# Optimization experiments

Hardware: AMD Instinct MI355X
Metric: run time of the kernel (lower is better)

## Reference

```python
import jax, jax.numpy as jnp
import numpy as np

B, N, M, CIN, COUT = 16, 512, 1024, 7, 64
C = CIN + 1  # density channel prepended
INIT_LS = 0.1


def setup_inputs() -> dict:
    key = jax.random.key(0)
    k1, k2, k3, k4 = jax.random.split(key, 4)
    context_in = jax.random.uniform(k1, (B, N, 1), dtype=jnp.float32)
    context_out = jax.random.normal(k2, (B, N, CIN), dtype=jnp.float32)
    target_in = jax.random.uniform(k3, (B, M, 1), dtype=jnp.float32)
    # learned params: sigma = log(init_length_scale) * ones(C); xavier-normal Linear
    sigma = jnp.full((C,), np.log(INIT_LS), dtype=jnp.float32)
    xavier_std = float(np.sqrt(2.0 / (C + COUT)))
    W = jax.random.normal(k4, (COUT, C), dtype=jnp.float32) * xavier_std
    b = jnp.zeros((COUT,), dtype=jnp.float32)
    return {"context_in": context_in, "context_out": context_out,
            "target_in": target_in, "sigma": sigma, "W": W, "b": b}


def reference(context_in, context_out, target_in, sigma, W, b):
    # pairwise squared distances over the 1-d input location: (B, N, M)
    dists = jnp.sum((context_in[:, :, None, :] - target_in[:, None, :, :]) ** 2, axis=-1)
    scales = jnp.exp(sigma)  # (C,)
    # per-channel RBF weights: (B, N, M, C)
    weights = jnp.exp(-0.5 * dists[..., None] / (scales ** 2))
    # prepend density channel of ones: (B, N, C)
    ctx = jnp.concatenate([jnp.ones(context_out.shape[:2] + (1,), context_out.dtype),
                           context_out], axis=-1)
    # weighted sum over context points N: (B, M, C)
    output = jnp.einsum('bnc,bnmc->bmc', ctx, weights)
    density, conv = output[..., :1], output[..., 1:]
    conv = conv / (density + 1e-8)
    output = jnp.concatenate([density, conv], axis=-1)
    # final linear projection (B, M, COUT)
    return jnp.einsum('bmc,oc->bmo', output, W) + b
```

## Files before the change

kernel.cpp:

```cpp
#include <hip/hip_runtime.h>


namespace {
constexpr int Bc    = 16;
constexpr int Nc    = 512;
constexpr int Mc    = 1024;
constexpr int CINc  = 7;
constexpr int Cc    = 8;
constexpr int CP    = 9;
constexpr int COUTc = 64;
constexpr int TM    = 32;
constexpr int NCH   = 16;
constexpr int NPC   = Nc / NCH;
constexpr int THREADS = TM * NCH;
constexpr float LOG2E = 1.4426950408889634f;
}

__global__ __launch_bounds__(THREADS) void convdeepset_kernel(
    const float* __restrict__ context_in,
    const float* __restrict__ context_out,
    const float* __restrict__ target_in,
    const float* __restrict__ sigma,
    const float* __restrict__ W,
    const float* __restrict__ bias,
    float* __restrict__ out)
{
    __shared__ float s_ctx[Nc * Cc];
    __shared__ float s_red[NCH][TM][CP];
    __shared__ float s_tot[TM][Cc];
    __shared__ float s_f[TM][Cc];
    __shared__ float s_Wt[Cc][COUTc];
    __shared__ float s_bias[COUTc];
    __shared__ float s_k2[Cc];

    const int t   = threadIdx.x;
    const int blk = blockIdx.x;
    const int b   = blk / (Mc / TM);
    const int m0  = (blk % (Mc / TM)) * TM;

    if (t < COUTc) s_bias[t] = bias[t];
    if (t < Cc) {
        float s = sigma[t];
        float inv_sc2 = __builtin_amdgcn_exp2f(-2.0f * s * LOG2E);
        s_k2[t] = -0.5f * inv_sc2 * LOG2E;
    }
    if (t < COUTc * Cc) {
        int o = t / Cc, c = t % Cc;
        s_Wt[c][o] = W[t];
    }
    {
        const int n = t;
        s_ctx[n * Cc] = context_in[b * Nc + n];
    }
    #pragma unroll
    for (int r = 0; r < (Nc * CINc) / THREADS; r++) {
        int e = r * THREADS + t;
        int n = e / CINc, c = e % CINc;
        s_ctx[n * Cc + 1 + c] = context_out[b * Nc * CINc + e];
    }
    __syncthreads();

    const int mi  = t % TM;
    const int ncq = t / TM;
    const float ti = target_in[b * Mc + m0 + mi];

    float k2[Cc];
    #pragma unroll
    for (int c = 0; c < Cc; c++) k2[c] = s_k2[c];
    bool uniform = true;
    #pragma unroll
    for (int c = 1; c < Cc; c++) uniform = uniform && (k2[c] == k2[0]);

    float acc[Cc];
    #pragma unroll
    for (int c = 0; c < Cc; c++) acc[c] = 0.0f;

    const int nbase = ncq * NPC;
    if (uniform) {
        const float k0 = k2[0];
        #pragma unroll 8
        for (int j = 0; j < NPC; j++) {
            const float4* p = (const float4*)&s_ctx[(nbase + j) * Cc];
            const float4 c0 = p[0], c1 = p[1];
            const float diff = c0.x - ti;
            const float w = __builtin_amdgcn_exp2f((k0 * diff) * diff);
            acc[0] += w;
            acc[1] += c0.y * w; acc[2] += c0.z * w; acc[3] += c0.w * w;
            acc[4] += c1.x * w; acc[5] += c1.y * w; acc[6] += c1.z * w; acc[7] += c1.w * w;
        }
    } else {
        #pragma unroll 4
        for (int j = 0; j < NPC; j++) {
            const float4* p = (const float4*)&s_ctx[(nbase + j) * Cc];
            const float4 c0 = p[0], c1 = p[1];
            const float diff = c0.x - ti;
            const float d = diff * diff;
            acc[0] += __builtin_amdgcn_exp2f(k2[0] * d);
            acc[1] += c0.y * __builtin_amdgcn_exp2f(k2[1] * d);
            acc[2] += c0.z * __builtin_amdgcn_exp2f(k2[2] * d);
            acc[3] += c0.w * __builtin_amdgcn_exp2f(k2[3] * d);
            acc[4] += c1.x * __builtin_amdgcn_exp2f(k2[4] * d);
            acc[5] += c1.y * __builtin_amdgcn_exp2f(k2[5] * d);
            acc[6] += c1.z * __builtin_amdgcn_exp2f(k2[6] * d);
            acc[7] += c1.w * __builtin_amdgcn_exp2f(k2[7] * d);
        }
    }

    #pragma unroll
    for (int c = 0; c < Cc; c++) s_red[ncq][mi][c] = acc[c];
    __syncthreads();

    if (t < TM * Cc) {
        const int rmi = t >> 3;
        const int rc  = t & 7;
        float tot = 0.0f;
        #pragma unroll
        for (int k = 0; k < NCH; k++) tot += s_red[k][rmi][rc];
        s_tot[rmi][rc] = tot;
    }
    __syncthreads();
    if (t < TM * Cc) {
        const int rmi = t >> 3;
        const int rc  = t & 7;
        const float tot  = s_tot[rmi][rc];
        const float dens = s_tot[rmi][0];
        s_f[rmi][rc] = (rc == 0) ? tot : tot / (dens + 1e-8f);
    }
    __syncthreads();

    const long long obase = (long long)(b * Mc + m0) * COUTc;
    #pragma unroll
    for (int r = 0; r < (TM * COUTc) / THREADS; r++) {
        const int flat = r * THREADS + t;
        const int o    = flat % COUTc;
        const int rmi  = flat / COUTc;
        float v = s_bias[o];
        #pragma unroll
        for (int c = 0; c < Cc; c++) v += s_f[rmi][c] * s_Wt[c][o];
        out[obase + flat] = v;
    }
}

extern "C" void kernel_launch(void* const* d_in, const int* in_sizes, int n_in,
                              void* d_out, int out_size, void* d_ws, size_t ws_size,
                              hipStream_t stream) {
    const float* context_in  = (const float*)d_in[0];
    const float* context_out = (const float*)d_in[1];
    const float* target_in   = (const float*)d_in[2];
    const float* sigma       = (const float*)d_in[3];
    const float* W           = (const float*)d_in[4];
    const float* bias        = (const float*)d_in[5];
    float* out = (float*)d_out;

    const int grid = Bc * (Mc / TM);
    convdeepset_kernel<<<grid, THREADS, 0, stream>>>(
        context_in, context_out, target_in, sigma, W, bias, out);
}
```

Baseline: 69.94 us.

## Halve target tile, double context split, reduce partials with wave shuffles

Changes the block tile from 32 targets x 16 context chunks to 16 targets x 32 chunks, which doubles the grid to 1024 blocks, and adds a min-blocks occupancy hint to launch_bounds. The per-thread partial sums are now reduced across the four 16-lane groups of each wave with xor shuffles, so only one row per wave is written to shared memory and the final reduction loops over 8 waves instead of 16 chunks. Each block still loads the full per-batch context into LDS and recomputes W/bias staging, so the doubled grid doubles that staging work. Unroll factors are lowered to fit the register budget.

```diff
diff --git a/kernel.cpp b/kernel.cpp
--- a/kernel.cpp
+++ b/kernel.cpp
@@ -9,14 +9,15 @@
 constexpr int Cc    = 8;
 constexpr int CP    = 9;
 constexpr int COUTc = 64;
-constexpr int TM    = 32;
-constexpr int NCH   = 16;
+constexpr int TM    = 16;
+constexpr int NCH   = 32;
 constexpr int NPC   = Nc / NCH;
 constexpr int THREADS = TM * NCH;
+constexpr int NWAVES  = THREADS / 64;
 constexpr float LOG2E = 1.4426950408889634f;
 }
 
-__global__ __launch_bounds__(THREADS) void convdeepset_kernel(
+__global__ __launch_bounds__(THREADS, 8) void convdeepset_kernel(
     const float* __restrict__ context_in,
     const float* __restrict__ context_out,
     const float* __restrict__ target_in,
@@ -26,7 +27,7 @@
     float* __restrict__ out)
 {
     __shared__ float s_ctx[Nc * Cc];
-    __shared__ float s_red[NCH][TM][CP];
+    __shared__ float s_red[NWAVES][TM][CP];
     __shared__ float s_tot[TM][Cc];
     __shared__ float s_f[TM][Cc];
     __shared__ float s_Wt[Cc][COUTc];
@@ -44,14 +45,11 @@
         float inv_sc2 = __builtin_amdgcn_exp2f(-2.0f * s * LOG2E);
         s_k2[t] = -0.5f * inv_sc2 * LOG2E;
     }
-    if (t < COUTc * Cc) {
+    {
         int o = t / Cc, c = t % Cc;
         s_Wt[c][o] = W[t];
     }
-    {
-        const int n = t;
-        s_ctx[n * Cc] = context_in[b * Nc + n];
-    }
+    s_ctx[t * Cc] = context_in[b * Nc + t];
     #pragma unroll
     for (int r = 0; r < (Nc * CINc) / THREADS; r++) {
         int e = r * THREADS + t;
@@ -60,16 +58,14 @@
     }
     __syncthreads();
 
-    const int mi  = t % TM;
-    const int ncq = t / TM;
+    const int mi  = t & (TM - 1);
+    const int ncq = t >> 4;
     const float ti = target_in[b * Mc + m0 + mi];
 
-    float k2[Cc];
-    #pragma unroll
-    for (int c = 0; c < Cc; c++) k2[c] = s_k2[c];
+    const float k0 = s_k2[0];
     bool uniform = true;
     #pragma unroll
-    for (int c = 1; c < Cc; c++) uniform = uniform && (k2[c] == k2[0]);
+    for (int c = 1; c < Cc; c++) uniform = uniform && (s_k2[c] == k0);
 
     float acc[Cc];
     #pragma unroll
@@ -77,8 +73,7 @@
 
     const int nbase = ncq * NPC;
     if (uniform) {
-        const float k0 = k2[0];
-        #pragma unroll 8
+        #pragma unroll 4
         for (int j = 0; j < NPC; j++) {
             const float4* p = (const float4*)&s_ctx[(nbase + j) * Cc];
             const float4 c0 = p[0], c1 = p[1];
@@ -89,25 +84,36 @@
             acc[4] += c1.x * w; acc[5] += c1.y * w; acc[6] += c1.z * w; acc[7] += c1.w * w;
         }
     } else {
-        #pragma unroll 4
+        #pragma unroll 2
         for (int j = 0; j < NPC; j++) {
             const float4* p = (const float4*)&s_ctx[(nbase + j) * Cc];
             const float4 c0 = p[0], c1 = p[1];
             const float diff = c0.x - ti;
             const float d = diff * diff;
-            acc[0] += __builtin_amdgcn_exp2f(k2[0] * d);
-            acc[1] += c0.y * __builtin_amdgcn_exp2f(k2[1] * d);
-            acc[2] += c0.z * __builtin_amdgcn_exp2f(k2[2] * d);
-            acc[3] += c0.w * __builtin_amdgcn_exp2f(k2[3] * d);
-            acc[4] += c1.x * __builtin_amdgcn_exp2f(k2[4] * d);
-            acc[5] += c1.y * __builtin_amdgcn_exp2f(k2[5] * d);
-            acc[6] += c1.z * __builtin_amdgcn_exp2f(k2[6] * d);
-            acc[7] += c1.w * __builtin_amdgcn_exp2f(k2[7] * d);
+            acc[0] +=        __builtin_amdgcn_exp2f(s_k2[0] * d);
+            acc[1] += c0.y * __builtin_amdgcn_exp2f(s_k2[1] * d);
+            acc[2] += c0.z * __builtin_amdgcn_exp2f(s_k2[2] * d);
+            acc[3] += c0.w * __builtin_amdgcn_exp2f(s_k2[3] * d);
+            acc[4] += c1.x * __builtin_amdgcn_exp2f(s_k2[4] * d);
+            acc[5] += c1.y * __builtin_amdgcn_exp2f(s_k2[5] * d);
+            acc[6] += c1.z * __builtin_amdgcn_exp2f(s_k2[6] * d);
+            acc[7] += c1.w * __builtin_amdgcn_exp2f(s_k2[7] * d);
         }
     }
 
     #pragma unroll
-    for (int c = 0; c < Cc; c++) s_red[ncq][mi][c] = acc[c];
+    for (int c = 0; c < Cc; c++) {
+        acc[c] += __shfl_xor(acc[c], 16);
+        acc[c] += __shfl_xor(acc[c], 32);
+    }
+    {
+        const int lane = t & 63;
+        const int w    = t >> 6;
+        if (lane < TM) {
+            #pragma unroll
+            for (int c = 0; c < Cc; c++) s_red[w][lane][c] = acc[c];
+        }
+    }
     __syncthreads();
 
     if (t < TM * Cc) {
@@ -115,7 +121,7 @@
         const int rc  = t & 7;
         float tot = 0.0f;
         #pragma unroll
-        for (int k = 0; k < NCH; k++) tot += s_red[k][rmi][rc];
+        for (int k = 0; k < NWAVES; k++) tot += s_red[k][rmi][rc];
         s_tot[rmi][rc] = tot;
     }
     __syncthreads();
@@ -132,7 +138,7 @@
     #pragma unroll
     for (int r = 0; r < (TM * COUTc) / THREADS; r++) {
         const int flat = r * THREADS + t;
-        const int o    = flat % COUTc;
+        const int o    = flat & (COUTc - 1);
         const int rmi  = flat / COUTc;
         float v = s_bias[o];
         #pragma unroll
```

Result: slower. 72.03 us (+3.0%).
